# Kernel optimization log

Measured on AMD Instinct MI355X. Metric: run time of the kernel, lower is better.

## Reference

```python
import jax, jax.numpy as jnp
import numpy as np

QMAX = 127.0  # 8-bit narrow-range symmetric: values in [-127, 127]


def _quantize_per_tensor(t):
    """Symmetric per-tensor int8 quantization (narrow range, like Brevitas Int8*PerTensorFloat).
    Returns (int8 codes as int32 for matmul, float scale)."""
    scale = jnp.max(jnp.abs(t)) / QMAX
    q = jnp.clip(jnp.round(t / scale), -QMAX, QMAX).astype(jnp.int8)
    return q, scale


def setup_inputs() -> dict:
    key = jax.random.key(0)
    k_x, k_w, k_b = jax.random.split(key, 3)
    size_in, size_out, n = 1024, 1024, 32768
    x = jax.random.normal(k_x, (n, size_in), dtype=jnp.float32)
    # kaiming_uniform_(a=sqrt(5)) on [size_out, size_in] -> bound = 1/sqrt(size_in)
    bound = 1.0 / np.sqrt(size_in)
    weight = jax.random.uniform(k_w, (size_out, size_in), dtype=jnp.float32,
                                minval=-bound, maxval=bound)
    bias = jax.random.uniform(k_b, (size_out,), dtype=jnp.float32,
                              minval=-bound, maxval=bound)
    return {"x": x, "weight": weight, "bias": bias}


def reference(x, weight, bias):
    # Quantize activations and weights to int8 per-tensor symmetric.
    qx, sx = _quantize_per_tensor(x)        # [N, K] int8, scalar scale
    qw, sw = _quantize_per_tensor(weight)   # [M, K] int8, scalar scale
    # Approximate-multiplier GEMM modeled as exact int8 MAC with int32 accum
    # (mul8s_acc is the accurate 8-bit multiplier LUT).
    acc = jnp.matmul(qx.astype(jnp.int32), qw.astype(jnp.int32).T)  # [N, M] int32
    # Rescale: output / ((QMAX/input_scale) * (QMAX/weight_scale)) with
    # Brevitas scale conventions == acc * sx * sw here.
    out = acc.astype(jnp.float32) * (sx * sw)
    return out + bias
```

## Files before the change

### kernel.cpp

```cpp
#include <hip/hip_runtime.h>
#include <cstdint>
#include <cstddef>


typedef int v4i __attribute__((ext_vector_type(4)));

#define QMAXF 127.0f
#define KDIM 1024
#define MDIM 1024
#define NBX 512
#define NBW 32

__global__ __launch_bounds__(256) void absmax_partial(
    const float4* __restrict__ x, int nx4,
    const float4* __restrict__ w, int nw4,
    float* __restrict__ partials) {
  const int b = blockIdx.x;
  const bool isw = (b >= NBX);
  const float4* __restrict__ p = isw ? w : x;
  const int n4 = isw ? nw4 : nx4;
  const int nb = isw ? NBW : NBX;
  const int bb = isw ? (b - NBX) : b;
  const int stride = nb * 256;

  float m0 = 0.f, m1 = 0.f, m2 = 0.f, m3 = 0.f;
  int i = bb * 256 + threadIdx.x;
  for (; i + 3 * stride < n4; i += 4 * stride) {
    float4 v0 = p[i], v1 = p[i + stride], v2 = p[i + 2 * stride],
           v3 = p[i + 3 * stride];
    m0 = fmaxf(m0, fmaxf(fmaxf(fabsf(v0.x), fabsf(v0.y)),
                         fmaxf(fabsf(v0.z), fabsf(v0.w))));
    m1 = fmaxf(m1, fmaxf(fmaxf(fabsf(v1.x), fabsf(v1.y)),
                         fmaxf(fabsf(v1.z), fabsf(v1.w))));
    m2 = fmaxf(m2, fmaxf(fmaxf(fabsf(v2.x), fabsf(v2.y)),
                         fmaxf(fabsf(v2.z), fabsf(v2.w))));
    m3 = fmaxf(m3, fmaxf(fmaxf(fabsf(v3.x), fabsf(v3.y)),
                         fmaxf(fabsf(v3.z), fabsf(v3.w))));
  }
  for (; i < n4; i += stride) {
    float4 v = p[i];
    m0 = fmaxf(m0, fmaxf(fmaxf(fabsf(v.x), fabsf(v.y)),
                         fmaxf(fabsf(v.z), fabsf(v.w))));
  }
  float m = fmaxf(fmaxf(m0, m1), fmaxf(m2, m3));
  for (int off = 32; off; off >>= 1) m = fmaxf(m, __shfl_down(m, off, 64));
  __shared__ float wm[4];
  const int lane = threadIdx.x & 63, wid = threadIdx.x >> 6;
  if (lane == 0) wm[wid] = m;
  __syncthreads();
  if (threadIdx.x == 0)
    partials[b] = fmaxf(fmaxf(wm[0], wm[1]), fmaxf(wm[2], wm[3]));
}

__global__ __launch_bounds__(256) void quant2(
    const float4* __restrict__ x, int nx16,
    const float4* __restrict__ w, int nw16,
    const float* __restrict__ partials,
    v4i* __restrict__ qx, v4i* __restrict__ qw,
    float* __restrict__ amax_out) {
  const int sel = blockIdx.y;
  const float* pp = partials + (sel ? NBX : 0);
  const int np = sel ? NBW : NBX;
  float m = 0.f;
  for (int i = threadIdx.x; i < np; i += 256) m = fmaxf(m, pp[i]);
  for (int off = 32; off; off >>= 1) m = fmaxf(m, __shfl_down(m, off, 64));
  __shared__ float wm[4];
  __shared__ float bmax;
  const int lane = threadIdx.x & 63, wid = threadIdx.x >> 6;
  if (lane == 0) wm[wid] = m;
  __syncthreads();
  if (threadIdx.x == 0) {
    float bm = fmaxf(fmaxf(wm[0], wm[1]), fmaxf(wm[2], wm[3]));
    bmax = bm;
    if (blockIdx.x == 0) amax_out[sel] = bm;
  }
  __syncthreads();
  const float amax = bmax;
  const float r = QMAXF / amax;

  const float4* __restrict__ p = sel ? w : x;
  const int n16 = sel ? nw16 : nx16;
  v4i* __restrict__ q = sel ? qw : qx;

  for (int i = blockIdx.x * 256 + threadIdx.x; i < n16;
       i += gridDim.x * 256) {
    float4 v0 = p[4 * i], v1 = p[4 * i + 1], v2 = p[4 * i + 2],
           v3 = p[4 * i + 3];
    v4i o;
#define QPK(V)                                                         \
  ((((int)fminf(fmaxf(rintf((V).x * r), -QMAXF), QMAXF)) & 255) |      \
   ((((int)fminf(fmaxf(rintf((V).y * r), -QMAXF), QMAXF)) & 255) << 8) | \
   ((((int)fminf(fmaxf(rintf((V).z * r), -QMAXF), QMAXF)) & 255) << 16) | \
   ((((int)fminf(fmaxf(rintf((V).w * r), -QMAXF), QMAXF)) & 255) << 24))
    o[0] = QPK(v0);
    o[1] = QPK(v1);
    o[2] = QPK(v2);
    o[3] = QPK(v3);
#undef QPK
    q[i] = o;
  }
}


__device__ __forceinline__ void ld_lds16(const void* g, void* l) {
  __builtin_amdgcn_global_load_lds(
      (__attribute__((address_space(1))) void*)(void*)g,
      (__attribute__((address_space(3))) void*)l, 16, 0, 0);
}

#define SBAR() asm volatile("s_barrier" ::: "memory")
#define WAITV(n) asm volatile("s_waitcnt vmcnt(" #n ")" ::: "memory")

#define BK 128
#define BMT 256
#define BNT 256

__global__ __launch_bounds__(512, 2) void gemm_i8(
    const char* __restrict__ qx, const char* __restrict__ qw,
    const float* __restrict__ bias, const float* __restrict__ amax,
    float* __restrict__ out) {
  __shared__ __align__(16) char smA[2][BNT * BK];
  __shared__ __align__(16) char smB[2][BMT * BK];

  const int tid = threadIdx.x;
  const int wave = tid >> 6;
  const int lane = tid & 63;

  const int p = blockIdx.x;
  const int lb = (p & 7) * 64 + (p >> 3);
  const int bm = lb >> 7;
  const int bn = lb & 127;

  const int wn = wave >> 1;
  const int wm = wave & 1;

  const char* __restrict__ xb = qx + (size_t)bn * BNT * KDIM;
  const char* __restrict__ wb = qw + (size_t)bm * BMT * KDIM;

  const int lrow = lane >> 3;
  const int sgx = (lane & 7) ^ lrow;
  const int gcol = sgx * 16;

  v4i acc[4][8] = {};

#define STAGE_A(bufc, kb, half) do {                                        \
    _Pragma("unroll") for (int c = 0; c < 2; ++c) {                         \
      const int sg = wave * 2 + c;                                          \
      const int rb = (sg >> 2) * 64 + (half) * 32 + (sg & 3) * 8;           \
      ld_lds16(xb + (size_t)(rb + lrow) * KDIM + (kb) + gcol,               \
               &smA[bufc][rb * BK]);                                        \
    }                                                                       \
  } while (0)
#define STAGE_B(bufc, kb, half) do {                                        \
    _Pragma("unroll") for (int c = 0; c < 2; ++c) {                         \
      const int sg = wave * 2 + c;                                          \
      const int rb = (sg >> 3) * 128 + (half) * 64 + (sg & 7) * 8;          \
      ld_lds16(wb + (size_t)(rb + lrow) * KDIM + (kb) + gcol,               \
               &smB[bufc][rb * BK]);                                        \
    }                                                                       \
  } while (0)

#define PHASE(bufc, ih, jh, STG, WT) do {                                   \
    v4i a_[2][2], b_[2][4];                                                 \
    _Pragma("unroll") for (int ks = 0; ks < 2; ++ks) {                      \
      const int sw = ((ks * 4 + (lane >> 4)) * 16) ^ ((lane & 7) * 16);     \
      _Pragma("unroll") for (int i = 0; i < 2; ++i) {                       \
        const int r = wn * 64 + (ih) * 32 + i * 16 + (lane & 15);           \
        a_[ks][i] = *(const v4i*)(&smA[bufc][r * BK + sw]);                 \
      }                                                                     \
      _Pragma("unroll") for (int j = 0; j < 4; ++j) {                       \
        const int r = wm * 128 + (jh) * 64 + j * 16 + (lane & 15);          \
        b_[ks][j] = *(const v4i*)(&smB[bufc][r * BK + sw]);                 \
      }                                                                     \
    }                                                                       \
    STG;                                                                    \
    WT;                                                                     \
    SBAR();                                                                 \
    __builtin_amdgcn_s_setprio(1);                                          \
    _Pragma("unroll") for (int ks = 0; ks < 2; ++ks)                        \
      _Pragma("unroll") for (int i = 0; i < 2; ++i)                         \
        _Pragma("unroll") for (int j = 0; j < 4; ++j)                       \
          acc[(ih) * 2 + i][(jh) * 4 + j] =                                 \
              __builtin_amdgcn_mfma_i32_16x16x64_i8(                        \
                  a_[ks][i], b_[ks][j], acc[(ih) * 2 + i][(jh) * 4 + j],    \
                  0, 0, 0);                                                 \
    __builtin_amdgcn_s_setprio(0);                                          \
  } while (0)

#define GROUP(bufc, kb1)                                                    \
    PHASE(bufc, 0, 0, STAGE_A((bufc) ^ 1, kb1, 0), WAITV(4));               \
    PHASE(bufc, 0, 1, STAGE_B((bufc) ^ 1, kb1, 0), WAITV(4));               \
    PHASE(bufc, 1, 0, STAGE_B((bufc) ^ 1, kb1, 1), (void)0);                \
    PHASE(bufc, 1, 1, STAGE_A((bufc) ^ 1, kb1, 1), WAITV(4));

  STAGE_A(0, 0, 0);
  STAGE_B(0, 0, 0);
  STAGE_B(0, 0, 1);
  STAGE_A(0, 0, 1);
  WAITV(4);
  SBAR();

  GROUP(0, 1 * BK);
  GROUP(1, 2 * BK);
  GROUP(0, 3 * BK);
  GROUP(1, 4 * BK);
  GROUP(0, 5 * BK);
  GROUP(1, 6 * BK);
  GROUP(0, 7 * BK);
  PHASE(1, 0, 0, (void)0, WAITV(2));
  PHASE(1, 0, 1, (void)0, WAITV(0));
  PHASE(1, 1, 0, (void)0, (void)0);
  PHASE(1, 1, 1, (void)0, (void)0);

#undef GROUP
#undef PHASE
#undef STAGE_A
#undef STAGE_B

  const float sfac = (amax[0] / QMAXF) * (amax[1] / QMAXF);
  const int mcol = bm * BMT + wm * 128 + (lane & 15);
  const int nb0 = bn * BNT + wn * 64 + ((lane >> 4) << 2);
  float bv[8];
#pragma unroll
  for (int j = 0; j < 8; ++j) bv[j] = bias[mcol + j * 16];
#pragma unroll
  for (int i = 0; i < 4; ++i) {
#pragma unroll
    for (int r = 0; r < 4; ++r) {
      const int n = nb0 + i * 16 + r;
      float* orow = out + (size_t)n * MDIM + mcol;
#pragma unroll
      for (int j = 0; j < 8; ++j)
        orow[j * 16] = (float)acc[i][j][r] * sfac + bv[j];
    }
  }
}

extern "C" void kernel_launch(void* const* d_in, const int* in_sizes, int n_in,
                              void* d_out, int out_size, void* d_ws, size_t ws_size,
                              hipStream_t stream) {
  const float* x = (const float*)d_in[0];
  const float* w = (const float*)d_in[1];
  const float* bias = (const float*)d_in[2];
  float* out = (float*)d_out;

  const int NX = in_sizes[0];
  const int NW = in_sizes[1];
  const int N = NX / KDIM;

  float* amax = (float*)d_ws;
  float* partials = (float*)((char*)d_ws + 64);
  char* qx = (char*)d_ws + 4096;
  char* qw = qx + (size_t)NX;

  absmax_partial<<<NBX + NBW, 256, 0, stream>>>(
      (const float4*)x, NX / 4, (const float4*)w, NW / 4, partials);

  dim3 qgrid(1024, 2);
  quant2<<<qgrid, 256, 0, stream>>>((const float4*)x, NX / 16,
                                    (const float4*)w, NW / 16, partials,
                                    (v4i*)qx, (v4i*)qw, amax);

  gemm_i8<<<dim3(512), 512, 0, stream>>>(qx, qw, bias, amax, out);
}
```

Before: 292.6 us.

## Switch int8 GEMM to 32x32x32 MFMA with two-phase K-tile pipeline

```diff
diff --git a/kernel.cpp b/kernel.cpp
--- a/kernel.cpp
+++ b/kernel.cpp
@@ -4,6 +4,7 @@
 
 
 typedef int v4i __attribute__((ext_vector_type(4)));
+typedef int v16i __attribute__((ext_vector_type(16)));
 
 #define QMAXF 127.0f
 #define KDIM 1024
@@ -110,6 +111,7 @@
 
 #define SBAR() asm volatile("s_barrier" ::: "memory")
 #define WAITV(n) asm volatile("s_waitcnt vmcnt(" #n ")" ::: "memory")
+#define WAITVLG() asm volatile("s_waitcnt vmcnt(0) lgkmcnt(0)" ::: "memory")
 
 #define BK 128
 #define BMT 256
@@ -140,37 +142,35 @@
   const int lrow = lane >> 3;
   const int sgx = (lane & 7) ^ lrow;
   const int gcol = sgx * 16;
-
-  v4i acc[4][8] = {};
-
-#define STAGE_A(bufc, kb, half) do {                                        \
-    _Pragma("unroll") for (int c = 0; c < 2; ++c) {                         \
-      const int sg = wave * 2 + c;                                          \
-      const int rb = (sg >> 2) * 64 + (half) * 32 + (sg & 3) * 8;           \
+  const int l31 = lane & 31;
+  const int lhi = lane >> 5;
+
+  v16i acc[2][4] = {};
+
+#define STAGE8(bufc, kb) do {                                               \
+    _Pragma("unroll") for (int c = 0; c < 4; ++c) {                         \
+      const int rb = (wave * 4 + c) * 8;                                    \
+      ld_lds16(wb + (size_t)(rb + lrow) * KDIM + (kb) + gcol,               \
+               &smB[bufc][rb * BK]);                                        \
+    }                                                                       \
+    _Pragma("unroll") for (int c = 0; c < 4; ++c) {                         \
+      const int rb = (wave * 4 + c) * 8;                                    \
       ld_lds16(xb + (size_t)(rb + lrow) * KDIM + (kb) + gcol,               \
                &smA[bufc][rb * BK]);                                        \
     }                                                                       \
   } while (0)
-#define STAGE_B(bufc, kb, half) do {                                        \
-    _Pragma("unroll") for (int c = 0; c < 2; ++c) {                         \
-      const int sg = wave * 2 + c;                                          \
-      const int rb = (sg >> 3) * 128 + (half) * 64 + (sg & 7) * 8;          \
-      ld_lds16(wb + (size_t)(rb + lrow) * KDIM + (kb) + gcol,               \
-               &smB[bufc][rb * BK]);                                        \
-    }                                                                       \
-  } while (0)
-
-#define PHASE(bufc, ih, jh, STG, WT) do {                                   \
+
+#define PHASE(bufc, ph, STG, WT) do {                                       \
     v4i a_[2][2], b_[2][4];                                                 \
     _Pragma("unroll") for (int ks = 0; ks < 2; ++ks) {                      \
-      const int sw = ((ks * 4 + (lane >> 4)) * 16) ^ ((lane & 7) * 16);     \
+      const int s = ((ph) * 2 + ks) * 2 + lhi;            \
       _Pragma("unroll") for (int i = 0; i < 2; ++i) {                       \
-        const int r = wn * 64 + (ih) * 32 + i * 16 + (lane & 15);           \
-        a_[ks][i] = *(const v4i*)(&smA[bufc][r * BK + sw]);                 \
+        const int r = wn * 64 + i * 32 + l31;                               \
+        a_[ks][i] = *(const v4i*)(&smA[bufc][r * BK + ((s ^ (r & 7)) * 16)]);\
       }                                                                     \
       _Pragma("unroll") for (int j = 0; j < 4; ++j) {                       \
-        const int r = wm * 128 + (jh) * 64 + j * 16 + (lane & 15);          \
-        b_[ks][j] = *(const v4i*)(&smB[bufc][r * BK + sw]);                 \
+        const int r = wm * 128 + j * 32 + l31;                              \
+        b_[ks][j] = *(const v4i*)(&smB[bufc][r * BK + ((s ^ (r & 7)) * 16)]);\
       }                                                                     \
     }                                                                       \
     STG;                                                                    \
@@ -180,58 +180,48 @@
     _Pragma("unroll") for (int ks = 0; ks < 2; ++ks)                        \
       _Pragma("unroll") for (int i = 0; i < 2; ++i)                         \
         _Pragma("unroll") for (int j = 0; j < 4; ++j)                       \
-          acc[(ih) * 2 + i][(jh) * 4 + j] =                                 \
-              __builtin_amdgcn_mfma_i32_16x16x64_i8(                        \
-                  a_[ks][i], b_[ks][j], acc[(ih) * 2 + i][(jh) * 4 + j],    \
-                  0, 0, 0);                                                 \
+          acc[i][j] = __builtin_amdgcn_mfma_i32_32x32x32_i8(                \
+              a_[ks][i], b_[ks][j], acc[i][j], 0, 0, 0);                    \
     __builtin_amdgcn_s_setprio(0);                                          \
   } while (0)
 
-#define GROUP(bufc, kb1)                                                    \
-    PHASE(bufc, 0, 0, STAGE_A((bufc) ^ 1, kb1, 0), WAITV(4));               \
-    PHASE(bufc, 0, 1, STAGE_B((bufc) ^ 1, kb1, 0), WAITV(4));               \
-    PHASE(bufc, 1, 0, STAGE_B((bufc) ^ 1, kb1, 1), (void)0);                \
-    PHASE(bufc, 1, 1, STAGE_A((bufc) ^ 1, kb1, 1), WAITV(4));
-
-  STAGE_A(0, 0, 0);
-  STAGE_B(0, 0, 0);
-  STAGE_B(0, 0, 1);
-  STAGE_A(0, 0, 1);
-  WAITV(4);
+#define TILE(bufc, kb1)                                                     \
+    PHASE(bufc, 0, STAGE8((bufc) ^ 1, kb1), (void)0);                       \
+    PHASE(bufc, 1, (void)0, WAITVLG());
+
+  STAGE8(0, 0);
+  WAITV(0);
   SBAR();
 
-  GROUP(0, 1 * BK);
-  GROUP(1, 2 * BK);
-  GROUP(0, 3 * BK);
-  GROUP(1, 4 * BK);
-  GROUP(0, 5 * BK);
-  GROUP(1, 6 * BK);
-  GROUP(0, 7 * BK);
-  PHASE(1, 0, 0, (void)0, WAITV(2));
-  PHASE(1, 0, 1, (void)0, WAITV(0));
-  PHASE(1, 1, 0, (void)0, (void)0);
-  PHASE(1, 1, 1, (void)0, (void)0);
-
-#undef GROUP
+  TILE(0, 1 * BK);
+  TILE(1, 2 * BK);
+  TILE(0, 3 * BK);
+  TILE(1, 4 * BK);
+  TILE(0, 5 * BK);
+  TILE(1, 6 * BK);
+  TILE(0, 7 * BK);
+  PHASE(1, 0, (void)0, (void)0);
+  PHASE(1, 1, (void)0, (void)0);
+
+#undef TILE
 #undef PHASE
-#undef STAGE_A
-#undef STAGE_B
+#undef STAGE8
 
   const float sfac = (amax[0] / QMAXF) * (amax[1] / QMAXF);
-  const int mcol = bm * BMT + wm * 128 + (lane & 15);
-  const int nb0 = bn * BNT + wn * 64 + ((lane >> 4) << 2);
-  float bv[8];
-#pragma unroll
-  for (int j = 0; j < 8; ++j) bv[j] = bias[mcol + j * 16];
-#pragma unroll
-  for (int i = 0; i < 4; ++i) {
-#pragma unroll
-    for (int r = 0; r < 4; ++r) {
-      const int n = nb0 + i * 16 + r;
+  const int mcol = bm * BMT + wm * 128 + l31;
+  const int nb0 = bn * BNT + wn * 64 + 4 * lhi;
+  float bv[4];
+#pragma unroll
+  for (int j = 0; j < 4; ++j) bv[j] = bias[mcol + j * 32];
+#pragma unroll
+  for (int i = 0; i < 2; ++i) {
+#pragma unroll
+    for (int r = 0; r < 16; ++r) {
+      const int n = nb0 + i * 32 + (r & 3) + 8 * (r >> 2);
       float* orow = out + (size_t)n * MDIM + mcol;
 #pragma unroll
-      for (int j = 0; j < 8; ++j)
-        orow[j * 16] = (float)acc[i][j][r] * sfac + bv[j];
+      for (int j = 0; j < 4; ++j)
+        orow[j * 32] = (float)acc[i][j][r] * sfac + bv[j];
     }
   }
 }
```

Measured after the change: 295.2 us. About the same (+0.9%).
